# Kernel optimization log

Measured on AMD Instinct MI355X. Metric: run time of the kernel, lower is better.

Reference implementation:

```python
import jax, jax.numpy as jnp
import numpy as np

T, D, E, K = 16384, 4096, 64, 2


def setup_inputs() -> dict:
    key = jax.random.key(0)
    k1, k2, k3 = jax.random.split(key, 3)
    x = jax.random.normal(k1, (T, D), dtype=jnp.float32)
    # torch nn.Linear default init scale ~ 1/sqrt(fan_in)
    gate_w = jax.random.normal(k2, (E, D), dtype=jnp.float32) * (1.0 / np.sqrt(D))
    gate_b = jax.random.normal(k3, (E,), dtype=jnp.float32) * (1.0 / np.sqrt(D))
    return {"x": x, "gate_w": gate_w, "gate_b": gate_b}


def reference(x, gate_w, gate_b):
    # gate linear: [T, D] @ [D, E] + [E] -> [T, E]
    router_logits = jnp.einsum("td,ed->te", x, gate_w) + gate_b
    # softmax over experts in float32 (matches F.softmax(..., dtype=torch.float))
    router_probs = jax.nn.softmax(router_logits.astype(jnp.float32), axis=-1)
    # top-k experts per token
    router_weights, select_expert_indices = jax.lax.top_k(router_probs, K)  # [T, K]
    # renormalize selected weights to sum to 1
    router_weights = router_weights / jnp.sum(router_weights, axis=-1, keepdims=True)
    router_weights = router_weights.astype(x.dtype)
    # one-hot mask [T, K, E] -> permute(2,1,0) -> [E, K, T]
    expert_mask = jax.nn.one_hot(select_expert_indices, E, dtype=jnp.int32)
    expert_mask = jnp.transpose(expert_mask, (2, 1, 0))
    return (router_logits, router_weights, select_expert_indices, expert_mask)
```

## Files before the change

kernel.cpp:

```cpp
#include <hip/hip_runtime.h>
#include <math.h>

#define T_TOK 16384
#define D_DIM 4096
#define E_EXP 64

#define OFF_W   (T_TOK * E_EXP)
#define OFF_I   (OFF_W + T_TOK * 2)
#define OFF_M   (OFF_I + T_TOK * 2)

#define NCHUNK    64
#define CH_HALVES 4096

typedef _Float16 half8 __attribute__((ext_vector_type(8)));
typedef float    f32x4 __attribute__((ext_vector_type(4)));

__global__ __launch_bounds__(256) void prep_w(const float* __restrict__ w,
                                              _Float16* __restrict__ ws_hi,
                                              _Float16* __restrict__ ws_lo) {
  const int g   = blockIdx.x * 256 + threadIdx.x;
  const int exp = g >> 8;
  const int kb  = (g & 255) * 16;
  const float* src = w + (size_t)exp * D_DIM + kb;
  float vals[16];
#pragma unroll
  for (int i = 0; i < 4; i++) {
    const float4 f = *(const float4*)(src + i * 4);
    vals[i * 4 + 0] = f.x; vals[i * 4 + 1] = f.y;
    vals[i * 4 + 2] = f.z; vals[i * 4 + 3] = f.w;
  }
  const int n_tile = exp >> 4, nn = exp & 15;
#pragma unroll
  for (int part = 0; part < 2; part++) {
    const int k0 = kb + part * 8;
    const int c = k0 >> 6, rem = k0 & 63;
    const int s = rem >> 5, q = (rem >> 3) & 3;
    const size_t off = (size_t)c * CH_HALVES + (n_tile * 2 + s) * 512 + (nn + 16 * q) * 8;
    half8 hv, lv;
#pragma unroll
    for (int j = 0; j < 8; j++) {
      const float xf = vals[part * 8 + j];
      const _Float16 h = (_Float16)xf;
      hv[j] = h;
      lv[j] = (_Float16)((xf - (float)h) * 2048.0f);
    }
    *(half8*)(ws_hi + off) = hv;
    *(half8*)(ws_lo + off) = lv;
  }
}

__global__ __launch_bounds__(256) void moe_mfma(
    const float* __restrict__ x, const _Float16* __restrict__ ws_hi,
    const _Float16* __restrict__ ws_lo, const float* __restrict__ bias,
    float* __restrict__ out) {
  const int tid  = threadIdx.x;
  const int wave = tid >> 6;
  const int lane = tid & 63;
  const int m    = lane & 15;
  const int q    = lane >> 4;
  const int trowbase = blockIdx.x * 64 + wave * 16;
  const float* xrow = x + (size_t)(trowbase + m) * D_DIM + q * 8;

  f32x4 accm[4], accc[4];
#pragma unroll
  for (int t = 0; t < 4; t++) {
    accm[t] = (f32x4){0.f, 0.f, 0.f, 0.f};
    accc[t] = (f32x4){0.f, 0.f, 0.f, 0.f};
  }

  float4 abuf[4][2];
  uint4  bh[2][4], bl[2][4];

  auto aload = [&](int ks, int slot) {
    const float* p = xrow + (ks >> 1) * 64 + (ks & 1) * 32;
    abuf[slot][0] = *(const float4*)p;
    abuf[slot][1] = *(const float4*)(p + 4);
  };
  auto bload = [&](int ks, int pb) {
    const size_t base = (size_t)(ks >> 1) * CH_HALVES + (ks & 1) * 512 + lane * 8;
    const _Float16* ph = ws_hi + base;
    const _Float16* pl = ws_lo + base;
#pragma unroll
    for (int t = 0; t < 4; t++) {
      bh[pb][t] = *(const uint4*)(ph + t * 1024);
      bl[pb][t] = *(const uint4*)(pl + t * 1024);
    }
  };
  auto comp = [&](int slot, int pb) {
    const float4 f0 = abuf[slot][0], f1 = abuf[slot][1];
    const float vv[8] = {f0.x, f0.y, f0.z, f0.w, f1.x, f1.y, f1.z, f1.w};
    half8 ah, al;
#pragma unroll
    for (int j = 0; j < 8; j++) {
      const _Float16 h = (_Float16)vv[j];
      ah[j] = h;
      al[j] = (_Float16)((vv[j] - (float)h) * 2048.0f);
    }
#pragma unroll
    for (int t = 0; t < 4; t++) {
      const half8 bhv = *(const half8*)&bh[pb][t];
      const half8 blv = *(const half8*)&bl[pb][t];
      accm[t] = __builtin_amdgcn_mfma_f32_16x16x32_f16(ah, bhv, accm[t], 0, 0, 0);
      accc[t] = __builtin_amdgcn_mfma_f32_16x16x32_f16(ah, blv, accc[t], 0, 0, 0);
      accc[t] = __builtin_amdgcn_mfma_f32_16x16x32_f16(al, bhv, accc[t], 0, 0, 0);
    }
  };

  aload(0, 0); aload(1, 1); aload(2, 2); aload(3, 3);
  bload(0, 0); bload(1, 1);

#pragma unroll 1
  for (int ks = 0; ks < 128; ks += 2) {
    comp(ks & 3, 0);
    if (ks + 4 < 128) aload(ks + 4, (ks + 4) & 3);
    if (ks + 2 < 128) bload(ks + 2, 0);
    comp((ks + 1) & 3, 1);
    if (ks + 5 < 128) aload(ks + 5, (ks + 5) & 3);
    if (ks + 3 < 128) bload(ks + 3, 1);
  }

  const int cc = lane & 15;
  float fin[4][4];
#pragma unroll
  for (int t = 0; t < 4; t++) {
    const float bb = bias[t * 16 + cc];
#pragma unroll
    for (int r = 0; r < 4; r++)
      fin[t][r] = accm[t][r] + accc[t][r] * 4.8828125e-4f + bb;
  }
#pragma unroll
  for (int r = 0; r < 4; r++) {
    const int trow = trowbase + q * 4 + r;
#pragma unroll
    for (int t = 0; t < 4; t++)
      out[(size_t)trow * E_EXP + t * 16 + cc] = fin[t][r];
  }

#pragma unroll
  for (int r = 0; r < 4; r++) {
    float v1 = fin[0][r]; int i1 = cc;
    float v2 = -3.4e38f;  int i2 = 0;
#pragma unroll
    for (int t = 1; t < 4; t++) {
      const float vc = fin[t][r]; const int ic = t * 16 + cc;
      if (vc > v1)      { v2 = v1; i2 = i1; v1 = vc; i1 = ic; }
      else if (vc > v2) { v2 = vc; i2 = ic; }
    }
#pragma unroll
    for (int mk = 1; mk <= 8; mk <<= 1) {
      const float ov1 = __shfl_xor(v1, mk); const int oi1 = __shfl_xor(i1, mk);
      const float ov2 = __shfl_xor(v2, mk); const int oi2 = __shfl_xor(i2, mk);
      if ((ov1 > v1) || (ov1 == v1 && oi1 < i1)) {
        const bool s2 = (v1 > ov2) || (v1 == ov2 && i1 < oi2);
        v2 = s2 ? v1 : ov2; i2 = s2 ? i1 : oi2;
        v1 = ov1; i1 = oi1;
      } else {
        const bool s2 = (ov1 > v2) || (ov1 == v2 && oi1 < i2);
        v2 = s2 ? ov1 : v2; i2 = s2 ? oi1 : i2;
      }
    }
    if (cc == 0) {
      const int trow = trowbase + q * 4 + r;
      const float d  = expf(v2 - v1);
      const float w1 = 1.f / (1.f + d);
      out[OFF_W + trow * 2 + 0] = w1;
      out[OFF_W + trow * 2 + 1] = d * w1;
      out[OFF_I + trow * 2 + 0] = (float)i1;
      out[OFF_I + trow * 2 + 1] = (float)i2;
      out[OFF_M + (size_t)(i1 * 2 + 0) * T_TOK + trow] = 1.0f;
      out[OFF_M + (size_t)(i2 * 2 + 1) * T_TOK + trow] = 1.0f;
    }
  }
}

extern "C" void kernel_launch(void* const* d_in, const int* in_sizes, int n_in,
                              void* d_out, int out_size, void* d_ws, size_t ws_size,
                              hipStream_t stream) {
  const float* x    = (const float*)d_in[0];
  const float* w    = (const float*)d_in[1];
  const float* bias = (const float*)d_in[2];
  float* out = (float*)d_out;
  _Float16* ws_hi = (_Float16*)d_ws;
  _Float16* ws_lo = ws_hi + (size_t)NCHUNK * CH_HALVES;

  hipMemsetAsync(out + OFF_M, 0, (size_t)E_EXP * 2 * T_TOK * sizeof(float), stream);
  prep_w<<<E_EXP * D_DIM / (256 * 16), 256, 0, stream>>>(w, ws_hi, ws_lo);
  moe_mfma<<<T_TOK / 64, 256, 0, stream>>>(x, ws_hi, ws_lo, bias, out);
}
```

Measured before the change: 490.3 us.

## Split K dimension across two wave groups per block with LDS reduction

Doubles the block to 512 threads and has each half of the waves process half of the 4096-long reduction dimension for the same 64 token rows. The halves are then combined through a shared-memory partial-sum exchange before the top-k epilogue. This halves the serial K loop per wave and raises the number of waves in flight, aiming to hide global-load latency better in this bandwidth-bound GEMV-like kernel. The prefetch is also restructured to load whole 64-wide chunks (two MFMA k-steps) per stage. The cost is 32 KB of LDS per block, a barrier, extra register pressure from the larger double buffers, and idle upper waves during the epilogue.

Result: faster. 399.4 us (-18.5%).

```diff
diff --git a/kernel.cpp b/kernel.cpp
--- a/kernel.cpp
+++ b/kernel.cpp
@@ -49,17 +49,22 @@
   }
 }
 
-__global__ __launch_bounds__(256) void moe_mfma(
+__global__ __launch_bounds__(512, 2) void moe_mfma(
     const float* __restrict__ x, const _Float16* __restrict__ ws_hi,
     const _Float16* __restrict__ ws_lo, const float* __restrict__ bias,
     float* __restrict__ out) {
+  __shared__ float part[4 * 32 * 64];
+
   const int tid  = threadIdx.x;
-  const int wave = tid >> 6;
+  const int wv   = tid >> 6;
+  const int wg   = wv & 3;
+  const int h    = wv >> 2;
   const int lane = tid & 63;
   const int m    = lane & 15;
   const int q    = lane >> 4;
-  const int trowbase = blockIdx.x * 64 + wave * 16;
+  const int trowbase = blockIdx.x * 64 + wg * 16;
   const float* xrow = x + (size_t)(trowbase + m) * D_DIM + q * 8;
+  const int cbase = h * 32;
 
   f32x4 accm[4], accc[4];
 #pragma unroll
@@ -68,58 +73,86 @@
     accc[t] = (f32x4){0.f, 0.f, 0.f, 0.f};
   }
 
-  float4 abuf[4][2];
-  uint4  bh[2][4], bl[2][4];
-
-  auto aload = [&](int ks, int slot) {
-    const float* p = xrow + (ks >> 1) * 64 + (ks & 1) * 32;
-    abuf[slot][0] = *(const float4*)p;
-    abuf[slot][1] = *(const float4*)(p + 4);
-  };
-  auto bload = [&](int ks, int pb) {
-    const size_t base = (size_t)(ks >> 1) * CH_HALVES + (ks & 1) * 512 + lane * 8;
-    const _Float16* ph = ws_hi + base;
-    const _Float16* pl = ws_lo + base;
-#pragma unroll
-    for (int t = 0; t < 4; t++) {
-      bh[pb][t] = *(const uint4*)(ph + t * 1024);
-      bl[pb][t] = *(const uint4*)(pl + t * 1024);
-    }
-  };
-  auto comp = [&](int slot, int pb) {
-    const float4 f0 = abuf[slot][0], f1 = abuf[slot][1];
-    const float vv[8] = {f0.x, f0.y, f0.z, f0.w, f1.x, f1.y, f1.z, f1.w};
-    half8 ah, al;
-#pragma unroll
-    for (int j = 0; j < 8; j++) {
-      const _Float16 h = (_Float16)vv[j];
-      ah[j] = h;
-      al[j] = (_Float16)((vv[j] - (float)h) * 2048.0f);
-    }
-#pragma unroll
-    for (int t = 0; t < 4; t++) {
-      const half8 bhv = *(const half8*)&bh[pb][t];
-      const half8 blv = *(const half8*)&bl[pb][t];
-      accm[t] = __builtin_amdgcn_mfma_f32_16x16x32_f16(ah, bhv, accm[t], 0, 0, 0);
-      accc[t] = __builtin_amdgcn_mfma_f32_16x16x32_f16(ah, blv, accc[t], 0, 0, 0);
-      accc[t] = __builtin_amdgcn_mfma_f32_16x16x32_f16(al, bhv, accc[t], 0, 0, 0);
-    }
-  };
-
-  aload(0, 0); aload(1, 1); aload(2, 2); aload(3, 3);
-  bload(0, 0); bload(1, 1);
+  float4 A0[4], A1[4];
+  half8  B0h[2][4], B0l[2][4];
+  half8  B1h[2][4], B1l[2][4];
+
+#define LOADA(A, c_) do {                                                  \
+    const float* p_ = xrow + (c_) * 64;                                    \
+    A[0] = *(const float4*)(p_);      A[1] = *(const float4*)(p_ + 4);     \
+    A[2] = *(const float4*)(p_ + 32); A[3] = *(const float4*)(p_ + 36);    \
+  } while (0)
+
+#define LOADB(Bh, Bl, c_) do {                                             \
+    const _Float16* ph_ = ws_hi + (size_t)(c_) * CH_HALVES + lane * 8;     \
+    const _Float16* pl_ = ws_lo + (size_t)(c_) * CH_HALVES + lane * 8;     \
+    _Pragma("unroll") for (int s_ = 0; s_ < 2; s_++)                       \
+    { _Pragma("unroll") for (int t_ = 0; t_ < 4; t_++) {                   \
+        Bh[s_][t_] = *(const half8*)(ph_ + s_ * 512 + t_ * 1024);          \
+        Bl[s_][t_] = *(const half8*)(pl_ + s_ * 512 + t_ * 1024);          \
+    } }                                                                    \
+  } while (0)
+
+#define CVT8(ah_, al_, f0, f1) do {                                        \
+    const float vv_[8] = {f0.x, f0.y, f0.z, f0.w, f1.x, f1.y, f1.z, f1.w}; \
+    _Pragma("unroll") for (int j_ = 0; j_ < 8; j_++) {                     \
+      const _Float16 hh_ = (_Float16)vv_[j_];                              \
+      ah_[j_] = hh_;                                                       \
+      al_[j_] = (_Float16)((vv_[j_] - (float)hh_) * 2048.0f);              \
+    }                                                                      \
+  } while (0)
+
+#define COMP(A, Bh, Bl) do {                                               \
+    half8 ah0_, al0_, ah1_, al1_;                                          \
+    CVT8(ah0_, al0_, A[0], A[1]);                                          \
+    CVT8(ah1_, al1_, A[2], A[3]);                                          \
+    _Pragma("unroll") for (int t_ = 0; t_ < 4; t_++) {                     \
+      accm[t_] = __builtin_amdgcn_mfma_f32_16x16x32_f16(ah0_, Bh[0][t_], accm[t_], 0, 0, 0); \
+      accc[t_] = __builtin_amdgcn_mfma_f32_16x16x32_f16(ah0_, Bl[0][t_], accc[t_], 0, 0, 0); \
+      accc[t_] = __builtin_amdgcn_mfma_f32_16x16x32_f16(al0_, Bh[0][t_], accc[t_], 0, 0, 0); \
+    }                                                                      \
+    _Pragma("unroll") for (int t_ = 0; t_ < 4; t_++) {                     \
+      accm[t_] = __builtin_amdgcn_mfma_f32_16x16x32_f16(ah1_, Bh[1][t_], accm[t_], 0, 0, 0); \
+      accc[t_] = __builtin_amdgcn_mfma_f32_16x16x32_f16(ah1_, Bl[1][t_], accc[t_], 0, 0, 0); \
+      accc[t_] = __builtin_amdgcn_mfma_f32_16x16x32_f16(al1_, Bh[1][t_], accc[t_], 0, 0, 0); \
+    }                                                                      \
+  } while (0)
+
+  LOADA(A0, cbase);     LOADB(B0h, B0l, cbase);
+  LOADA(A1, cbase + 1); LOADB(B1h, B1l, cbase + 1);
 
 #pragma unroll 1
-  for (int ks = 0; ks < 128; ks += 2) {
-    comp(ks & 3, 0);
-    if (ks + 4 < 128) aload(ks + 4, (ks + 4) & 3);
-    if (ks + 2 < 128) bload(ks + 2, 0);
-    comp((ks + 1) & 3, 1);
-    if (ks + 5 < 128) aload(ks + 5, (ks + 5) & 3);
-    if (ks + 3 < 128) bload(ks + 3, 1);
-  }
-
-  const int cc = lane & 15;
+  for (int c = cbase; c < cbase + 32; c += 2) {
+    COMP(A0, B0h, B0l);
+    if (c + 2 < cbase + 32) { LOADA(A0, c + 2); LOADB(B0h, B0l, c + 2); }
+    COMP(A1, B1h, B1l);
+    if (c + 3 < cbase + 32) { LOADA(A1, c + 3); LOADB(B1h, B1l, c + 3); }
+  }
+
+  if (h == 1) {
+    float* pp = part + wg * 2048 + lane;
+#pragma unroll
+    for (int t = 0; t < 4; t++)
+#pragma unroll
+      for (int r = 0; r < 4; r++) {
+        pp[(t * 4 + r) * 64]        = accm[t][r];
+        pp[(16 + t * 4 + r) * 64]   = accc[t][r];
+      }
+  }
+  __syncthreads();
+  if (h == 1) return;
+  {
+    const float* pp = part + wg * 2048 + lane;
+#pragma unroll
+    for (int t = 0; t < 4; t++)
+#pragma unroll
+      for (int r = 0; r < 4; r++) {
+        accm[t][r] += pp[(t * 4 + r) * 64];
+        accc[t][r] += pp[(16 + t * 4 + r) * 64];
+      }
+  }
+
+  const int cc = m;
   float fin[4][4];
 #pragma unroll
   for (int t = 0; t < 4; t++) {
@@ -185,5 +218,5 @@
 
   hipMemsetAsync(out + OFF_M, 0, (size_t)E_EXP * 2 * T_TOK * sizeof(float), stream);
   prep_w<<<E_EXP * D_DIM / (256 * 16), 256, 0, stream>>>(w, ws_hi, ws_lo);
-  moe_mfma<<<T_TOK / 64, 256, 0, stream>>>(x, ws_hi, ws_lo, bias, out);
+  moe_mfma<<<T_TOK / 64, 512, 0, stream>>>(x, ws_hi, ws_lo, bias, out);
 }
```
